# Kernel tuning notes

Measured on AMD Instinct MI355X. Metric: run time of the kernel, lower is better.

The kernel has to match this reference:

```python
import jax, jax.numpy as jnp
import numpy as np

BS, N, H, F_IN, F_OUT = 4, 2048, 2, 768, 768
NEG_SLOPE = 0.2

def setup_inputs() -> dict:
    key = jax.random.key(0)
    k_h, k_adj, k_w, k_as, k_ad = jax.random.split(key, 5)
    h = jax.random.normal(k_h, (BS, N, F_IN), dtype=jnp.float32)
    adj = jax.random.randint(k_adj, (BS, N, N), 0, 2) > 0  # bool adjacency
    # xavier_uniform fan_in/fan_out per torch semantics on [H, f_in, f_out]
    limit_w = float(np.sqrt(6.0 / (F_IN + F_OUT)))
    w = jax.random.uniform(k_w, (H, F_IN, F_OUT), minval=-limit_w, maxval=limit_w, dtype=jnp.float32)
    limit_a = float(np.sqrt(6.0 / (F_OUT + 1)))
    a_src = jax.random.uniform(k_as, (H, F_OUT, 1), minval=-limit_a, maxval=limit_a, dtype=jnp.float32)
    a_dst = jax.random.uniform(k_ad, (H, F_OUT, 1), minval=-limit_a, maxval=limit_a, dtype=jnp.float32)
    bias = jnp.zeros((F_OUT,), dtype=jnp.float32)
    return {"h": h, "adj": adj, "w": w, "a_src": a_src, "a_dst": a_dst, "bias": bias}

def reference(h, adj, w, a_src, a_dst, bias):
    # h: [b, n, f_in]; w: [H, f_in, f_out] -> h_prime: [b, H, n, f_out]
    h_prime = jnp.einsum('bnf,hfo->bhno', h, w)
    t = jnp.tanh(h_prime)
    attn_src = jnp.einsum('bhno,ho->bhn', t, a_src[..., 0])  # [b, H, n]
    attn_dst = jnp.einsum('bhno,ho->bhn', t, a_dst[..., 0])  # [b, H, n]
    # broadcast add: scores[b,h,i,j] = src[i] + dst[j]
    attn = attn_src[:, :, :, None] + attn_dst[:, :, None, :]
    attn = jnp.where(attn >= 0, attn, NEG_SLOPE * attn)  # leaky_relu
    n = adj.shape[-1]
    keep = adj[:, None, :, :] | jnp.eye(n, dtype=bool)[None, None]  # [b,1,n,n]
    attn = jnp.where(keep, attn, -jnp.inf)
    attn = jax.nn.softmax(attn, axis=-1)
    # dropout is identity at inference
    out = jnp.einsum('bhij,bhjo->bhio', attn, h_prime)
    return out + bias
```

## Files before the change

### kernel.cpp

```cpp
#include <hip/hip_runtime.h>
#include <hip/hip_bf16.h>
#include <cstdint>
#include <cstddef>

#define BS   4
#define NN   2048
#define NH   2
#define FIN  768
#define FOUT 768
#define NEG_SLOPE 0.2f

typedef __attribute__((ext_vector_type(8))) short short8;
typedef __attribute__((ext_vector_type(4))) float float4v;

static __device__ __forceinline__ float bits2f(unsigned short u) {
    union { unsigned int i; float f; } v; v.i = ((unsigned int)u) << 16; return v.f;
}
static __device__ __forceinline__ unsigned short f2bits(float f) {
    union { float f; unsigned int i; } v; v.f = f;
    unsigned int x = v.i;
    unsigned int r = x + 0x7fffu + ((x >> 16) & 1u);
    return (unsigned short)(r >> 16);
}
static __device__ __forceinline__ float fast_tanh(float x) {
    float xc = fminf(fmaxf(x, -20.f), 20.f);
    float e = __expf(2.f * xc);
    return (e - 1.f) / (e + 1.f);
}
static __device__ __forceinline__ void async_copy16(void* lds, const void* g) {
    __builtin_amdgcn_global_load_lds(
        (const __attribute__((address_space(1))) unsigned int*)g,
        (__attribute__((address_space(3))) unsigned int*)lds, 16, 0, 0);
}

static __device__ __forceinline__ bool detect_isf32(const unsigned short* h_raw) {
    unsigned short u = h_raw[threadIdx.x & 63];
    int e = (u >> 7) & 0xFF;
    unsigned long long m = __ballot(e >= 118 && e <= 134);
    return __popcll(m) < 48;
}
static __device__ __forceinline__ bool detect_adj8(const unsigned char* adj_raw) {
    int l = threadIdx.x & 63;
    unsigned char v = (unsigned char)(adj_raw[l * 4 + 1] | adj_raw[l * 4 + 2] |
                                      adj_raw[l * 4 + 3]);
    unsigned long long m = __ballot(v != 0);
    return __popcll(m) > 8;
}

#define NB_H   3072
#define NB_W   1152
#define NB_Z   128
__global__ __launch_bounds__(256) void k_prep(
    const void* __restrict__ hr, unsigned short* __restrict__ h_bf,
    const void* __restrict__ wr, unsigned short* __restrict__ wt_b,
    const void* __restrict__ as_raw, const void* __restrict__ ad_raw,
    const void* __restrict__ b_raw,
    float* __restrict__ asf, float* __restrict__ adf, float* __restrict__ bff,
    float* __restrict__ attn_acc)
{
    __shared__ float tile[32][33];
    int bi = blockIdx.x;
    int t = threadIdx.x;
    if (bi < NB_H) {
        bool isf = detect_isf32((const unsigned short*)hr);
        int base = (bi * 256 + t) * 8;
        if (isf) {
            float4 f0 = *((const float4*)((const float*)hr + base));
            float4 f1 = *((const float4*)((const float*)hr + base + 4));
            unsigned short v[8] = { f2bits(f0.x), f2bits(f0.y), f2bits(f0.z), f2bits(f0.w),
                                    f2bits(f1.x), f2bits(f1.y), f2bits(f1.z), f2bits(f1.w) };
            *(uint4*)(h_bf + base) = *(const uint4*)v;
        } else {
            *(uint4*)(h_bf + base) = *(const uint4*)((const unsigned short*)hr + base);
        }
        return;
    }
    if (bi < NB_H + NB_W) {
        bool isf = detect_isf32((const unsigned short*)hr);
        int wb = bi - NB_H;
        int h  = wb / 576;
        int rem = wb % 576;
        int f0 = (rem % 24) * 32;
        int o0 = (rem / 24) * 32;
        int tx = t & 31, ty = t >> 5;
        #pragma unroll
        for (int r = 0; r < 4; ++r) {
            int fl = ty * 4 + r;
            size_t idx = (size_t)h * FIN * FOUT + (size_t)(f0 + fl) * FOUT + (o0 + tx);
            tile[fl][tx] = isf ? ((const float*)wr)[idx]
                               : bits2f(((const unsigned short*)wr)[idx]);
        }
        __syncthreads();
        #pragma unroll
        for (int r = 0; r < 4; ++r) {
            int ol = ty * 4 + r;
            size_t oidx = (size_t)h * FOUT * FIN + (size_t)(o0 + ol) * FIN + (f0 + tx);
            wt_b[oidx] = f2bits(tile[tx][ol]);
        }
        return;
    }
    if (bi < NB_H + NB_W + NB_Z) {
        attn_acc[(bi - NB_H - NB_W) * 256 + t] = 0.f;
        return;
    }
    bool isf = detect_isf32((const unsigned short*)hr);
    for (int i = t; i < NH * FOUT; i += 256) {
        asf[i] = isf ? ((const float*)as_raw)[i] : bits2f(((const unsigned short*)as_raw)[i]);
        adf[i] = isf ? ((const float*)ad_raw)[i] : bits2f(((const unsigned short*)ad_raw)[i]);
    }
    for (int i = t; i < FOUT; i += 256)
        bff[i] = isf ? ((const float*)b_raw)[i] : bits2f(((const unsigned short*)b_raw)[i]);
}

#define BM 128
#define BN 128
#define BK 64
#define NXB (NN / BM)
#define NYB (FOUT / BN)
#define BLKS_PER_BATCH (NXB * NYB)
#define GEMM_GRID (BLKS_PER_BATCH * BS * NH)

__global__ __launch_bounds__(256) void k_gemm_hw(
    const unsigned short* __restrict__ hh,
    const unsigned short* __restrict__ wh,
    unsigned short* __restrict__ hpT,
    const float* __restrict__ asf, const float* __restrict__ adf,
    float* __restrict__ attn_src, float* __restrict__ attn_dst)
{
    int lid = blockIdx.x;
    int ib  = lid & 7;
    int rem = lid >> 3;
    int i0  = (rem & 15) * BM;
    int o0  = (rem >> 4) * BN;
    int b  = ib / NH, hd = ib % NH;
    const unsigned short* A  = hh + (size_t)b  * NN * FIN;
    const unsigned short* Bt = wh + (size_t)hd * FOUT * FIN;
    unsigned short*       C  = hpT + (size_t)ib * FOUT * NN;

    __shared__ __align__(16) unsigned short As[BM * BK];
    __shared__ __align__(16) unsigned short Bs[BN * BK];

    int t = threadIdx.x;
    int lane = t & 63, wave = t >> 6;
    int wm = (wave & 1) * 64, wn = (wave >> 1) * 64;
    int lm = lane & 15, quad = lane >> 4;
    int rr = lane >> 3;
    int cc = lane & 7;
    int gc = cc ^ rr;
    int e  = lm & 7;

    float4v acc[4][4] = {};

    for (int k0 = 0; k0 < FIN; k0 += BK) {
        __syncthreads();
        #pragma unroll
        for (int p = 0; p < 4; ++p) {
            int r0 = wave * 32 + p * 8;
            async_copy16(&As[r0 * BK], A  + (size_t)(i0 + r0 + rr) * FIN + k0 + gc * 8);
            async_copy16(&Bs[r0 * BK], Bt + (size_t)(o0 + r0 + rr) * FIN + k0 + gc * 8);
        }
        __syncthreads();
        #pragma unroll
        for (int kk = 0; kk < 2; ++kk) {
            int slot = ((kk << 2) | quad) ^ e;
            short8 fa[4], fb[4];
            #pragma unroll
            for (int mt = 0; mt < 4; ++mt)
                fa[mt] = *(const short8*)&As[(wm + mt * 16 + lm) * BK + slot * 8];
            #pragma unroll
            for (int nt = 0; nt < 4; ++nt)
                fb[nt] = *(const short8*)&Bs[(wn + nt * 16 + lm) * BK + slot * 8];
            #pragma unroll
            for (int mt = 0; mt < 4; ++mt)
                #pragma unroll
                for (int nt = 0; nt < 4; ++nt)
                    acc[mt][nt] = __builtin_amdgcn_mfma_f32_16x16x32_bf16(
                        fa[mt], fb[nt], acc[mt][nt], 0, 0, 0);
        }
    }

    float asv[4], adv[4];
    #pragma unroll
    for (int nt = 0; nt < 4; ++nt) {
        int o = o0 + wn + nt * 16 + lm;
        asv[nt] = asf[hd * FOUT + o];
        adv[nt] = adf[hd * FOUT + o];
    }
    #pragma unroll
    for (int mt = 0; mt < 4; ++mt) {
        float ps[4] = {0.f, 0.f, 0.f, 0.f};
        float pd[4] = {0.f, 0.f, 0.f, 0.f};
        #pragma unroll
        for (int nt = 0; nt < 4; ++nt) {
            int node = i0 + wm + mt * 16 + quad * 4;
            int o    = o0 + wn + nt * 16 + lm;
            ushort4 v;
            v.x = f2bits(acc[mt][nt][0]);
            v.y = f2bits(acc[mt][nt][1]);
            v.z = f2bits(acc[mt][nt][2]);
            v.w = f2bits(acc[mt][nt][3]);
            *(ushort4*)&C[(size_t)o * NN + node] = v;
            #pragma unroll
            for (int r = 0; r < 4; ++r) {
                float tv = fast_tanh(acc[mt][nt][r]);
                ps[r] += tv * asv[nt];
                pd[r] += tv * adv[nt];
            }
        }
        #pragma unroll
        for (int r = 0; r < 4; ++r) {
            float s = ps[r], d = pd[r];
            #pragma unroll
            for (int off = 1; off <= 8; off <<= 1) {
                s += __shfl_xor(s, off);
                d += __shfl_xor(d, off);
            }
            if (lm == 0) {
                int node = i0 + wm + mt * 16 + quad * 4 + r;
                atomicAdd(&attn_src[ib * NN + node], s);
                atomicAdd(&attn_dst[ib * NN + node], d);
            }
        }
    }
}

__global__ __launch_bounds__(256) void k_softmax_p(
    const float* __restrict__ attn_src, const float* __restrict__ attn_dst,
    const void* __restrict__ adj_raw,
    unsigned short* __restrict__ P)
{
    int blk = blockIdx.x;
    int i = blk & (NN - 1);
    int b = blk >> 11;
    bool is8 = detect_adj8((const unsigned char*)adj_raw);
    int t = threadIdx.x;
    int lane = t & 63, wave = t >> 6;
    int j0 = t * 8;

    bool keep[8];
    if (is8) {
        const unsigned char* arow = (const unsigned char*)adj_raw + ((size_t)b * NN + i) * NN;
        uint2 v = *(const uint2*)(arow + j0);
        #pragma unroll
        for (int r = 0; r < 8; ++r) {
            unsigned int w = (r < 4) ? v.x : v.y;
            keep[r] = ((w >> ((r & 3) * 8)) & 0xFFu) != 0;
        }
    } else {
        const int* arow = (const int*)adj_raw + ((size_t)b * NN + i) * NN;
        int4 v0 = *(const int4*)(arow + j0);
        int4 v1 = *(const int4*)(arow + j0 + 4);
        keep[0] = v0.x != 0; keep[1] = v0.y != 0; keep[2] = v0.z != 0; keep[3] = v0.w != 0;
        keep[4] = v1.x != 0; keep[5] = v1.y != 0; keep[6] = v1.z != 0; keep[7] = v1.w != 0;
    }
    #pragma unroll
    for (int r = 0; r < 8; ++r) keep[r] = keep[r] || (j0 + r == i);

    __shared__ float redm[NH][4], reds[NH][4];
    int bh0 = b * NH;
    float src0 = attn_src[(size_t)bh0 * NN + i];
    float src1 = attn_src[(size_t)(bh0 + 1) * NN + i];
    const float* drow0 = attn_dst + (size_t)bh0 * NN;
    const float* drow1 = attn_dst + (size_t)(bh0 + 1) * NN;
    float4 a0 = *(const float4*)(drow0 + j0);
    float4 a1 = *(const float4*)(drow0 + j0 + 4);
    float4 c0 = *(const float4*)(drow1 + j0);
    float4 c1 = *(const float4*)(drow1 + j0 + 4);
    float dj0[8] = { a0.x, a0.y, a0.z, a0.w, a1.x, a1.y, a1.z, a1.w };
    float dj1[8] = { c0.x, c0.y, c0.z, c0.w, c1.x, c1.y, c1.z, c1.w };

    float s0[8], s1[8];
    float lm0 = -1e30f, lm1 = -1e30f;
    #pragma unroll
    for (int r = 0; r < 8; ++r) {
        float sc0 = src0 + dj0[r];
        sc0 = sc0 >= 0.f ? sc0 : NEG_SLOPE * sc0;
        s0[r] = keep[r] ? sc0 : -1e30f;
        lm0 = fmaxf(lm0, s0[r]);
        float sc1 = src1 + dj1[r];
        sc1 = sc1 >= 0.f ? sc1 : NEG_SLOPE * sc1;
        s1[r] = keep[r] ? sc1 : -1e30f;
        lm1 = fmaxf(lm1, s1[r]);
    }
    #pragma unroll
    for (int off = 32; off > 0; off >>= 1) {
        lm0 = fmaxf(lm0, __shfl_xor(lm0, off));
        lm1 = fmaxf(lm1, __shfl_xor(lm1, off));
    }
    if (lane == 0) { redm[0][wave] = lm0; redm[1][wave] = lm1; }
    __syncthreads();
    float m0 = fmaxf(fmaxf(redm[0][0], redm[0][1]), fmaxf(redm[0][2], redm[0][3]));
    float m1 = fmaxf(fmaxf(redm[1][0], redm[1][1]), fmaxf(redm[1][2], redm[1][3]));

    float p0[8], p1[8];
    float ls0 = 0.f, ls1 = 0.f;
    #pragma unroll
    for (int r = 0; r < 8; ++r) {
        p0[r] = __expf(s0[r] - m0); ls0 += p0[r];
        p1[r] = __expf(s1[r] - m1); ls1 += p1[r];
    }
    #pragma unroll
    for (int off = 32; off > 0; off >>= 1) {
        ls0 += __shfl_xor(ls0, off);
        ls1 += __shfl_xor(ls1, off);
    }
    if (lane == 0) { reds[0][wave] = ls0; reds[1][wave] = ls1; }
    __syncthreads();
    float inv0 = 1.0f / (reds[0][0] + reds[0][1] + reds[0][2] + reds[0][3]);
    float inv1 = 1.0f / (reds[1][0] + reds[1][1] + reds[1][2] + reds[1][3]);

    uint4 pw;
    pw.x = ((unsigned int)f2bits(p0[1] * inv0) << 16) | f2bits(p0[0] * inv0);
    pw.y = ((unsigned int)f2bits(p0[3] * inv0) << 16) | f2bits(p0[2] * inv0);
    pw.z = ((unsigned int)f2bits(p0[5] * inv0) << 16) | f2bits(p0[4] * inv0);
    pw.w = ((unsigned int)f2bits(p0[7] * inv0) << 16) | f2bits(p0[6] * inv0);
    *(uint4*)&P[((size_t)bh0 * NN + i) * NN + j0] = pw;
    pw.x = ((unsigned int)f2bits(p1[1] * inv1) << 16) | f2bits(p1[0] * inv1);
    pw.y = ((unsigned int)f2bits(p1[3] * inv1) << 16) | f2bits(p1[2] * inv1);
    pw.z = ((unsigned int)f2bits(p1[5] * inv1) << 16) | f2bits(p1[4] * inv1);
    pw.w = ((unsigned int)f2bits(p1[7] * inv1) << 16) | f2bits(p1[6] * inv1);
    *(uint4*)&P[((size_t)(bh0 + 1) * NN + i) * NN + j0] = pw;
}

#define BM2 256
#define BN2 192
#define BK2 64
#define NT2 (NN / BK2)
#define GRID2 (8 * (NN / BM2) * (FOUT / BN2))

__global__ __launch_bounds__(512, 2) void k_gemm_out(
    const unsigned short* __restrict__ P,
    const unsigned short* __restrict__ hpT,
    const float* __restrict__ bf,
    void* __restrict__ outp, const unsigned short* __restrict__ h_raw)
{
    bool isf = detect_isf32(h_raw);
    int lid = blockIdx.x;
    int ib  = lid & 7;
    int rem = lid >> 3;
    int i0  = (rem & 7) * BM2;
    int o0  = (rem >> 3) * BN2;
    const unsigned short* A  = P   + (size_t)ib * NN * NN;
    const unsigned short* Bt = hpT + (size_t)ib * FOUT * NN;

    __shared__ __align__(16) unsigned short As[3][BM2 * BK2];
    __shared__ __align__(16) unsigned short Bs[2][BN2 * BK2];

    int t = threadIdx.x;
    int lane = t & 63, wave = t >> 6;
    int wr = wave >> 2, wc = wave & 3;
    int wm = wr * 128, wn = wc * 48;
    int lm = lane & 15, quad = lane >> 4;
    int e  = lm & 7;
    int rr = lane >> 3, cc = lane & 7, gc = cc ^ rr;

    float4v acc[8][3] = {};

    auto stageA = [&](int slot, int q, int kt) {
        int r0 = q * 64 + wave * 8;
        async_copy16(&As[slot][r0 * BK2],
                     A + (size_t)(i0 + r0 + rr) * NN + kt * BK2 + gc * 8);
    };
    auto stageB = [&](int slot, int q, int kt) {
        int r0 = q * 64 + wave * 8;
        async_copy16(&Bs[slot][r0 * BK2],
                     Bt + (size_t)(o0 + r0 + rr) * NN + kt * BK2 + gc * 8);
    };

    stageA(0, 0, 0); stageA(0, 1, 0); stageA(0, 2, 0); stageA(0, 3, 0);
    stageB(0, 0, 0); stageB(0, 1, 0); stageB(0, 2, 0);
    stageA(1, 0, 1); stageA(1, 1, 1); stageA(1, 2, 1); stageA(1, 3, 1);
    asm volatile("s_waitcnt vmcnt(4)" ::: "memory");
    __builtin_amdgcn_s_barrier();

    short8 fa[2][2];
    short8 fb[3][2];

    int sr = 0;
    for (int u = 0; u < NT2; ++u) {
        int sw = sr + 2; if (sw >= 3) sw -= 3;
        int sbw = (u + 1) & 1;
        bool moreA = (u < NT2 - 2);
        bool moreB = (u < NT2 - 1);
        const unsigned short* Ac = As[sr];
        const unsigned short* Bc = Bs[u & 1];

        if (moreB) { stageB(sbw, 0, u + 1); stageB(sbw, 1, u + 1); stageB(sbw, 2, u + 1); }
        if (moreA) { stageA(sw, 0, u + 2); stageA(sw, 1, u + 2);
                     stageA(sw, 2, u + 2); stageA(sw, 3, u + 2); }

        #pragma unroll
        for (int nt = 0; nt < 3; ++nt)
            #pragma unroll
            for (int kk = 0; kk < 2; ++kk)
                fb[nt][kk] = *(const short8*)&Bc[(wn + nt * 16 + lm) * BK2 +
                                                 ((((kk << 2) | quad) ^ e) * 8)];

        __builtin_amdgcn_s_setprio(1);
        #pragma unroll
        for (int g = 0; g < 4; ++g) {
            #pragma unroll
            for (int mt = 0; mt < 2; ++mt)
                #pragma unroll
                for (int kk = 0; kk < 2; ++kk)
                    fa[mt][kk] = *(const short8*)&Ac[(wm + g * 32 + mt * 16 + lm) * BK2 +
                                                     ((((kk << 2) | quad) ^ e) * 8)];
            #pragma unroll
            for (int mt = 0; mt < 2; ++mt)
                #pragma unroll
                for (int nt = 0; nt < 3; ++nt)
                    #pragma unroll
                    for (int kk = 0; kk < 2; ++kk)
                        acc[2 * g + mt][nt] = __builtin_amdgcn_mfma_f32_16x16x32_bf16(
                            fa[mt][kk], fb[nt][kk], acc[2 * g + mt][nt], 0, 0, 0);
        }
        __builtin_amdgcn_s_setprio(0);

        if (moreA)      asm volatile("s_waitcnt vmcnt(4)" ::: "memory");
        else if (moreB) asm volatile("s_waitcnt vmcnt(0)" ::: "memory");
        __builtin_amdgcn_s_barrier();

        sr = sr + 1 == 3 ? 0 : sr + 1;
    }

    if (isf) {
        float* C = (float*)outp + (size_t)ib * NN * FOUT;
        #pragma unroll
        for (int nt = 0; nt < 3; ++nt) {
            int o = o0 + wn + nt * 16 + lm;
            float bv = bf[o];
            #pragma unroll
            for (int mt = 0; mt < 8; ++mt) {
                int i = i0 + wm + mt * 16 + quad * 4;
                #pragma unroll
                for (int r = 0; r < 4; ++r)
                    C[(size_t)(i + r) * FOUT + o] = acc[mt][nt][r] + bv;
            }
        }
    } else {
        unsigned short* C = (unsigned short*)outp + (size_t)ib * NN * FOUT;
        #pragma unroll
        for (int nt = 0; nt < 3; ++nt) {
            int o = o0 + wn + nt * 16 + lm;
            float bv = bf[o];
            #pragma unroll
            for (int mt = 0; mt < 8; ++mt) {
                int i = i0 + wm + mt * 16 + quad * 4;
                #pragma unroll
                for (int r = 0; r < 4; ++r)
                    C[(size_t)(i + r) * FOUT + o] = f2bits(acc[mt][nt][r] + bv);
            }
        }
    }
}

extern "C" void kernel_launch(void* const* d_in, const int* in_sizes, int n_in,
                              void* d_out, int out_size, void* d_ws, size_t ws_size,
                              hipStream_t stream)
{
    const void* h_raw   = d_in[0];
    const void* adj_raw = d_in[1];
    const void* w_raw   = d_in[2];
    const void* as_raw  = d_in[3];
    const void* ad_raw  = d_in[4];
    const void* b_raw   = d_in[5];

    char* ws = (char*)d_ws;
    size_t off = 0;
    unsigned short* hpT = (unsigned short*)(ws + off); off += (size_t)BS * NH * FOUT * NN * 2;
    float* asr = (float*)(ws + off);            off += (size_t)BS * NH * NN * 4;
    float* ads = (float*)(ws + off);            off += (size_t)BS * NH * NN * 4;
    size_t uoff = off;
    unsigned short* P    = (unsigned short*)(ws + uoff);
    unsigned short* h_bf = (unsigned short*)(ws + uoff); uoff += (size_t)BS * NN * FIN * 2;
    unsigned short* wt_b = (unsigned short*)(ws + uoff); uoff += (size_t)NH * FOUT * FIN * 2;
    off += (size_t)BS * NH * NN * NN * 2;
    float* asf = (float*)(ws + off);            off += (size_t)NH * FOUT * 4;
    float* adf = (float*)(ws + off);            off += (size_t)NH * FOUT * 4;
    float* bff = (float*)(ws + off);            off += 4096;

    k_prep<<<NB_H + NB_W + NB_Z + 1, 256, 0, stream>>>(
        h_raw, h_bf, w_raw, wt_b, as_raw, ad_raw, b_raw, asf, adf, bff, asr);
    k_gemm_hw<<<dim3(GEMM_GRID), 256, 0, stream>>>(
        h_bf, wt_b, hpT, asf, adf, asr, ads);
    k_softmax_p<<<dim3(BS * NN), 256, 0, stream>>>(asr, ads, adj_raw, P);
    k_gemm_out<<<dim3(GRID2), 512, 0, stream>>>(
        P, hpT, bff, d_out, (const unsigned short*)h_raw);
}
```

Before: 267.6 us.

## Double waves per output GEMM block with producer waves and split-phase pipelining

The output GEMM block grows from 512 to 1024 threads. Each wave now covers 64 rows instead of 128, halving its accumulator tiles. Only the first 8 waves issue the async global-to-LDS copies, and the A-tile staging is split into two halves between two MFMA phases, with extra barriers in between. The intent is more waves in flight to hide LDS and memory latency, at the cost of more barrier synchronisation and a tighter register budget from the new launch bounds, which could cause spills.

```diff
diff --git a/kernel.cpp b/kernel.cpp
--- a/kernel.cpp
+++ b/kernel.cpp
@@ -328,7 +328,7 @@
 #define NT2 (NN / BK2)
 #define GRID2 (8 * (NN / BM2) * (FOUT / BN2))
 
-__global__ __launch_bounds__(512, 2) void k_gemm_out(
+__global__ __launch_bounds__(1024, 4) void k_gemm_out(
     const unsigned short* __restrict__ P,
     const unsigned short* __restrict__ hpT,
     const float* __restrict__ bf,
@@ -349,12 +349,13 @@
     int t = threadIdx.x;
     int lane = t & 63, wave = t >> 6;
     int wr = wave >> 2, wc = wave & 3;
-    int wm = wr * 128, wn = wc * 48;
+    int wm = wr * 64, wn = wc * 48;
     int lm = lane & 15, quad = lane >> 4;
     int e  = lm & 7;
     int rr = lane >> 3, cc = lane & 7, gc = cc ^ rr;
-
-    float4v acc[8][3] = {};
+    bool prod = (wave < 8);
+
+    float4v acc[4][3] = {};
 
     auto stageA = [&](int slot, int q, int kt) {
         int r0 = q * 64 + wave * 8;
@@ -367,9 +368,11 @@
                      Bt + (size_t)(o0 + r0 + rr) * NN + kt * BK2 + gc * 8);
     };
 
-    stageA(0, 0, 0); stageA(0, 1, 0); stageA(0, 2, 0); stageA(0, 3, 0);
-    stageB(0, 0, 0); stageB(0, 1, 0); stageB(0, 2, 0);
-    stageA(1, 0, 1); stageA(1, 1, 1); stageA(1, 2, 1); stageA(1, 3, 1);
+    if (prod) {
+        stageA(0, 0, 0); stageA(0, 1, 0); stageA(0, 2, 0); stageA(0, 3, 0);
+        stageB(0, 0, 0); stageB(0, 1, 0); stageB(0, 2, 0);
+        stageA(1, 0, 1); stageA(1, 1, 1); stageA(1, 2, 1); stageA(1, 3, 1);
+    }
     asm volatile("s_waitcnt vmcnt(4)" ::: "memory");
     __builtin_amdgcn_s_barrier();
 
@@ -385,37 +388,52 @@
         const unsigned short* Ac = As[sr];
         const unsigned short* Bc = Bs[u & 1];
 
-        if (moreB) { stageB(sbw, 0, u + 1); stageB(sbw, 1, u + 1); stageB(sbw, 2, u + 1); }
-        if (moreA) { stageA(sw, 0, u + 2); stageA(sw, 1, u + 2);
-                     stageA(sw, 2, u + 2); stageA(sw, 3, u + 2); }
-
         #pragma unroll
         for (int nt = 0; nt < 3; ++nt)
             #pragma unroll
             for (int kk = 0; kk < 2; ++kk)
                 fb[nt][kk] = *(const short8*)&Bc[(wn + nt * 16 + lm) * BK2 +
                                                  ((((kk << 2) | quad) ^ e) * 8)];
-
+        #pragma unroll
+        for (int mt = 0; mt < 2; ++mt)
+            #pragma unroll
+            for (int kk = 0; kk < 2; ++kk)
+                fa[mt][kk] = *(const short8*)&Ac[(wm + mt * 16 + lm) * BK2 +
+                                                 ((((kk << 2) | quad) ^ e) * 8)];
+        if (prod && moreB) { stageB(sbw, 0, u + 1); stageB(sbw, 1, u + 1);
+                             stageB(sbw, 2, u + 1); }
+        if (prod && moreA) { stageA(sw, 0, u + 2); stageA(sw, 1, u + 2); }
+        __builtin_amdgcn_s_barrier();
         __builtin_amdgcn_s_setprio(1);
         #pragma unroll
-        for (int g = 0; g < 4; ++g) {
-            #pragma unroll
-            for (int mt = 0; mt < 2; ++mt)
+        for (int mt = 0; mt < 2; ++mt)
+            #pragma unroll
+            for (int nt = 0; nt < 3; ++nt)
                 #pragma unroll
                 for (int kk = 0; kk < 2; ++kk)
-                    fa[mt][kk] = *(const short8*)&Ac[(wm + g * 32 + mt * 16 + lm) * BK2 +
-                                                     ((((kk << 2) | quad) ^ e) * 8)];
-            #pragma unroll
-            for (int mt = 0; mt < 2; ++mt)
+                    acc[mt][nt] = __builtin_amdgcn_mfma_f32_16x16x32_bf16(
+                        fa[mt][kk], fb[nt][kk], acc[mt][nt], 0, 0, 0);
+        __builtin_amdgcn_s_setprio(0);
+        __builtin_amdgcn_s_barrier();
+
+        #pragma unroll
+        for (int mt = 0; mt < 2; ++mt)
+            #pragma unroll
+            for (int kk = 0; kk < 2; ++kk)
+                fa[mt][kk] = *(const short8*)&Ac[(wm + 32 + mt * 16 + lm) * BK2 +
+                                                 ((((kk << 2) | quad) ^ e) * 8)];
+        if (prod && moreA) { stageA(sw, 2, u + 2); stageA(sw, 3, u + 2); }
+        __builtin_amdgcn_s_barrier();
+        __builtin_amdgcn_s_setprio(1);
+        #pragma unroll
+        for (int mt = 0; mt < 2; ++mt)
+            #pragma unroll
+            for (int nt = 0; nt < 3; ++nt)
                 #pragma unroll
-                for (int nt = 0; nt < 3; ++nt)
-                    #pragma unroll
-                    for (int kk = 0; kk < 2; ++kk)
-                        acc[2 * g + mt][nt] = __builtin_amdgcn_mfma_f32_16x16x32_bf16(
-                            fa[mt][kk], fb[nt][kk], acc[2 * g + mt][nt], 0, 0, 0);
-        }
+                for (int kk = 0; kk < 2; ++kk)
+                    acc[2 + mt][nt] = __builtin_amdgcn_mfma_f32_16x16x32_bf16(
+                        fa[mt][kk], fb[nt][kk], acc[2 + mt][nt], 0, 0, 0);
         __builtin_amdgcn_s_setprio(0);
-
         if (moreA)      asm volatile("s_waitcnt vmcnt(4)" ::: "memory");
         else if (moreB) asm volatile("s_waitcnt vmcnt(0)" ::: "memory");
         __builtin_amdgcn_s_barrier();
@@ -430,7 +448,7 @@
             int o = o0 + wn + nt * 16 + lm;
             float bv = bf[o];
             #pragma unroll
-            for (int mt = 0; mt < 8; ++mt) {
+            for (int mt = 0; mt < 4; ++mt) {
                 int i = i0 + wm + mt * 16 + quad * 4;
                 #pragma unroll
                 for (int r = 0; r < 4; ++r)
@@ -444,7 +462,7 @@
             int o = o0 + wn + nt * 16 + lm;
             float bv = bf[o];
             #pragma unroll
-            for (int mt = 0; mt < 8; ++mt) {
+            for (int mt = 0; mt < 4; ++mt) {
                 int i = i0 + wm + mt * 16 + quad * 4;
                 #pragma unroll
                 for (int r = 0; r < 4; ++r)
@@ -484,6 +502,6 @@
     k_gemm_hw<<<dim3(GEMM_GRID), 256, 0, stream>>>(
         h_bf, wt_b, hpT, asf, adf, asr, ads);
     k_softmax_p<<<dim3(BS * NN), 256, 0, stream>>>(asr, ads, adj_raw, P);
-    k_gemm_out<<<dim3(GRID2), 512, 0, stream>>>(
+    k_gemm_out<<<dim3(GRID2), 1024, 0, stream>>>(
         P, hpT, bff, d_out, (const unsigned short*)h_raw);
 }
```

Measured after the change: 254.0 us. 5.1% less time.
